# Kernel optimization log

Hardware: AMD Instinct MI355X
Metric: run time of the kernel (lower is better)

Reference implementation:

```python
import jax, jax.numpy as jnp
import numpy as np

D = 1024
H = 16
HD = D // H

def setup_inputs() -> dict:
    key = jax.random.key(0)
    ks = jax.random.split(key, 5)
    scale = 1.0 / np.sqrt(D)
    x = jax.random.normal(ks[0], (2, 2048, D), dtype=jnp.float32)
    W_qkv = jax.random.uniform(ks[1], (D, 3 * D), minval=-scale, maxval=scale, dtype=jnp.float32)
    b_qkv = jax.random.uniform(ks[2], (3 * D,), minval=-scale, maxval=scale, dtype=jnp.float32)
    W_out = jax.random.uniform(ks[3], (D, D), minval=-scale, maxval=scale, dtype=jnp.float32)
    b_out = jax.random.uniform(ks[4], (D,), minval=-scale, maxval=scale, dtype=jnp.float32)
    return {"x": x, "W_qkv": W_qkv, "b_qkv": b_qkv, "W_out": W_out, "b_out": b_out}

def reference(x, W_qkv, b_qkv, W_out, b_out):
    B, S, _ = x.shape
    qkv = x @ W_qkv + b_qkv  # [B,S,3D]
    qkv = qkv.reshape(B, S, 3, H, HD).transpose(2, 0, 3, 1, 4)  # [3,B,H,S,HD]
    q, k, v = qkv[0], qkv[1], qkv[2]
    scores = jnp.einsum('bhsd,bhtd->bhst', q, k) / jnp.sqrt(jnp.float32(HD))
    probs = jax.nn.softmax(scores, axis=-1)
    attn = jnp.einsum('bhst,bhtd->bhsd', probs, v)  # [B,H,S,HD]
    attn = attn.transpose(0, 2, 1, 3).reshape(B, S, D)
    return attn @ W_out + b_out
```

## Files before the change

### kernel.cpp

```cpp
#include <hip/hip_runtime.h>


typedef short bf16x8 __attribute__((ext_vector_type(8)));
typedef short bf16x4 __attribute__((ext_vector_type(4)));
typedef float f32x4 __attribute__((ext_vector_type(4)));

#if __has_builtin(__builtin_amdgcn_mfma_f32_16x16x16_bf16)
#define MFMA16(a, b, c) __builtin_amdgcn_mfma_f32_16x16x16_bf16(a, b, c, 0, 0, 0)
#else
#define MFMA16(a, b, c) __builtin_amdgcn_mfma_f32_16x16x16bf16_1k(a, b, c, 0, 0, 0)
#endif

__device__ __forceinline__ unsigned short f2bf(float f) {
  unsigned u = __float_as_uint(f);
  u = (u + 0x7fffu + ((u >> 16) & 1u)) >> 16;
  return (unsigned short)u;
}
__device__ __forceinline__ unsigned pack_bf2(float lo, float hi) {
  unsigned a = __float_as_uint(lo) + 0x8000u;
  unsigned b = __float_as_uint(hi) + 0x8000u;
  return __builtin_amdgcn_perm(b, a, 0x07060302);
}
__device__ __forceinline__ void load_lds16(const unsigned short* g, unsigned short* l) {
  __builtin_amdgcn_global_load_lds(
      (const __attribute__((address_space(1))) void*)g,
      (__attribute__((address_space(3))) void*)l, 16, 0, 0);
}

__global__ __launch_bounds__(256) void prep(
    const float* __restrict__ x, unsigned short* __restrict__ x_bf,
    const float* __restrict__ W_qkv, unsigned short* __restrict__ Wqkv_t,
    const float* __restrict__ W_out, unsigned short* __restrict__ Wout_t)
{
  const int tid = threadIdx.x;
  if (blockIdx.z == 2) {
    const int bid = blockIdx.y * 48 + blockIdx.x;
    const int n = 4096 * 1024;
    for (int i = bid * 2048 + tid * 8; i < n; i += 768 * 2048) {
      float4 f0 = *(const float4*)(x + i);
      float4 f1 = *(const float4*)(x + i + 4);
      union { unsigned short u[8]; uint4 v; } pk;
      pk.u[0] = f2bf(f0.x); pk.u[1] = f2bf(f0.y); pk.u[2] = f2bf(f0.z); pk.u[3] = f2bf(f0.w);
      pk.u[4] = f2bf(f1.x); pk.u[5] = f2bf(f1.y); pk.u[6] = f2bf(f1.z); pk.u[7] = f2bf(f1.w);
      *(uint4*)(x_bf + i) = pk.v;
    }
    return;
  }
  const float* in = (blockIdx.z == 0) ? W_qkv : W_out;
  unsigned short* out = (blockIdx.z == 0) ? Wqkv_t : Wout_t;
  const int R = 1024;
  const int C = (blockIdx.z == 0) ? 3072 : 1024;
  const int c0 = blockIdx.x * 64;
  if (c0 >= C) return;
  __shared__ float tile[64][65];
  const int r0 = blockIdx.y * 64;
  {
    const int rr = tid >> 4;
    const int cc = (tid & 15) * 4;
#pragma unroll
    for (int it = 0; it < 4; ++it) {
      float4 f = *(const float4*)&in[(size_t)(r0 + rr + 16 * it) * C + c0 + cc];
      tile[rr + 16 * it][cc + 0] = f.x;
      tile[rr + 16 * it][cc + 1] = f.y;
      tile[rr + 16 * it][cc + 2] = f.z;
      tile[rr + 16 * it][cc + 3] = f.w;
    }
  }
  __syncthreads();
  {
    const int cr = tid >> 2;
    const int rk = (tid & 3) * 16;
    union { unsigned short u[16]; uint4 v[2]; } pk;
#pragma unroll
    for (int j = 0; j < 16; ++j) pk.u[j] = f2bf(tile[rk + j][cr]);
    uint4* dst = (uint4*)&out[(size_t)(c0 + cr) * R + r0 + rk];
    dst[0] = pk.v[0];
    dst[1] = pk.v[1];
  }
}

template <int MODE>
__global__ __launch_bounds__(256) void gemm_mfma(
    const unsigned short* __restrict__ A,
    const unsigned short* __restrict__ Bt,
    const float* __restrict__ bias,
    void* __restrict__ Cout, unsigned short* __restrict__ vT,
    int M, int N, int K, int ldc)
{
  __shared__ unsigned short As[128][32];
  __shared__ unsigned short Bs[128][32];
  const int tid = threadIdx.x;
  const int wave = tid >> 6, lane = tid & 63;
  const int l16 = lane & 15, quad = lane >> 4;
  const int m0 = blockIdx.y * 128, n0 = blockIdx.x * 128;
  const int wm = (wave & 1) * 64, wn = (wave >> 1) * 64;
  const int lr = lane >> 2;
  const int lc = (lane & 3) * 8;

  f32x4 acc[4][4] = {};

  for (int k0 = 0; k0 < K; k0 += 32) {
    __syncthreads();
    load_lds16(&A [(size_t)(m0 + 16 * wave + lr) * K + k0 + lc],      &As[16 * wave][0]);
    load_lds16(&A [(size_t)(m0 + 64 + 16 * wave + lr) * K + k0 + lc], &As[64 + 16 * wave][0]);
    load_lds16(&Bt[(size_t)(n0 + 16 * wave + lr) * K + k0 + lc],      &Bs[16 * wave][0]);
    load_lds16(&Bt[(size_t)(n0 + 64 + 16 * wave + lr) * K + k0 + lc], &Bs[64 + 16 * wave][0]);
    __syncthreads();

    bf16x8 af[4], bfr[4];
#pragma unroll
    for (int mi = 0; mi < 4; ++mi)
      af[mi] = *(const bf16x8*)&As[wm + 16 * mi + l16][quad * 8];
#pragma unroll
    for (int ni = 0; ni < 4; ++ni)
      bfr[ni] = *(const bf16x8*)&Bs[wn + 16 * ni + l16][quad * 8];
#pragma unroll
    for (int mi = 0; mi < 4; ++mi)
#pragma unroll
      for (int ni = 0; ni < 4; ++ni)
        acc[mi][ni] = __builtin_amdgcn_mfma_f32_16x16x32_bf16(
            af[mi], bfr[ni], acc[mi][ni], 0, 0, 0);
  }

  const float SCQ = 0.18033688f;
#pragma unroll
  for (int ni = 0; ni < 4; ++ni) {
    const int colb = n0 + wn + 16 * ni;
    const int col = colb + l16;
    const float bv = bias[col];
    if (MODE == 0) {
#pragma unroll
      for (int mi = 0; mi < 4; ++mi)
#pragma unroll
        for (int i = 0; i < 4; ++i) {
          const int row = m0 + wm + 16 * mi + quad * 4 + i;
          ((float*)Cout)[(size_t)row * ldc + col] = acc[mi][ni][i] + bv;
        }
    } else if (colb < 1024) {
#pragma unroll
      for (int mi = 0; mi < 4; ++mi)
#pragma unroll
        for (int i = 0; i < 4; ++i) {
          const int row = m0 + wm + 16 * mi + quad * 4 + i;
          ((unsigned short*)Cout)[(size_t)row * ldc + col] = f2bf((acc[mi][ni][i] + bv) * SCQ);
        }
    } else if (colb < 2048) {
#pragma unroll
      for (int mi = 0; mi < 4; ++mi)
#pragma unroll
        for (int i = 0; i < 4; ++i) {
          const int row = m0 + wm + 16 * mi + quad * 4 + i;
          ((unsigned short*)Cout)[(size_t)row * ldc + col] = f2bf(acc[mi][ni][i] + bv);
        }
    } else {
      const int h = (col - 2048) >> 6, d = col & 63;
#pragma unroll
      for (int mi = 0; mi < 4; ++mi) {
        const int row = m0 + wm + 16 * mi + quad * 4;
        const int bb = row >> 11, t = row & 2047;
        unsigned short* dst = &vT[((size_t)(bb * 16 + h) * 64 + d) * 2048 + t];
        *(unsigned*)(dst)     = pack_bf2(acc[mi][ni][0] + bv, acc[mi][ni][1] + bv);
        *(unsigned*)(dst + 2) = pack_bf2(acc[mi][ni][2] + bv, acc[mi][ni][3] + bv);
      }
    }
  }
}

__global__ __launch_bounds__(256, 2) void attn_mfma(
    const unsigned short* __restrict__ qk,
    const unsigned short* __restrict__ vT,
    unsigned short* __restrict__ attn_out)
{
  __shared__ unsigned short Ks[2][4096];
  __shared__ unsigned short Vs[2][4096];

  const int tid = threadIdx.x;
  const int wave = tid >> 6, lane = tid & 63;
  const int l16 = lane & 15, quad = lane >> 4;
  const int bh = blockIdx.y, b = bh >> 4, h = bh & 15;
  const int s0 = blockIdx.x * 128 + wave * 32;

  const unsigned short* qb = qk + (size_t)(b * 2048) * 2048 + h * 64;
  const unsigned short* kb = qb + 1024;
  const unsigned short* vb = vT + (size_t)bh * 64 * 2048;

  const int srow = lane >> 3;
  const int schunk = ((lane & 7) ^ srow) * 8;
  const int r0a = wave * 16;
  const unsigned short* kg0 = kb + (size_t)(r0a + srow) * 2048 + schunk;
  const unsigned short* kg1 = kg0 + (size_t)8 * 2048;
  const unsigned short* vg0 = vb + (size_t)(r0a + srow) * 2048 + schunk;
  const unsigned short* vg1 = vg0 + (size_t)8 * 2048;
  const int wd0 = r0a * 64 + lane * 8;
  const int wd1 = (r0a + 8) * 64 + lane * 8;

  uint4 kr0 = *(const uint4*)(kg0);
  uint4 kr1 = *(const uint4*)(kg1);
  uint4 vr0 = *(const uint4*)(vg0);
  uint4 vr1 = *(const uint4*)(vg1);
  *(uint4*)&Ks[0][wd0] = kr0;  *(uint4*)&Ks[0][wd1] = kr1;
  *(uint4*)&Vs[0][wd0] = vr0;  *(uint4*)&Vs[0][wd1] = vr1;
  kr0 = *(const uint4*)(kg0 + (size_t)64 * 2048);
  kr1 = *(const uint4*)(kg1 + (size_t)64 * 2048);
  vr0 = *(const uint4*)(vg0 + 64);
  vr1 = *(const uint4*)(vg1 + 64);

  bf16x8 qf[2][2];
#pragma unroll
  for (int mt = 0; mt < 2; ++mt)
#pragma unroll
    for (int ks = 0; ks < 2; ++ks)
      qf[mt][ks] = *(const bf16x8*)&qb[(size_t)(s0 + 16 * mt + l16) * 2048 + 32 * ks + quad * 8];

  f32x4 O[2][4] = {};
  f32x4 lacc[2] = {};
  const bf16x4 ones4 = {(short)0x3F80, (short)0x3F80, (short)0x3F80, (short)0x3F80};
  const int sw = l16 & 7;
  const int h2 = quad >> 1, h1 = (quad & 1) * 4;

  __syncthreads();

  for (int it = 0; it < 32; ++it) {
    const int cur = it & 1;

    bf16x8 kf[4][2];
#pragma unroll
    for (int nt = 0; nt < 4; ++nt) {
      const int rb = (16 * nt + l16) * 64;
      kf[nt][0] = *(const bf16x8*)&Ks[cur][rb + ((quad ^ sw) * 8)];
      kf[nt][1] = *(const bf16x8*)&Ks[cur][rb + (((4 + quad) ^ sw) * 8)];
    }

    f32x4 sf[4][2];
#pragma unroll
    for (int nt = 0; nt < 4; ++nt)
#pragma unroll
      for (int mt = 0; mt < 2; ++mt) {
        f32x4 c = {0.0f, 0.0f, 0.0f, 0.0f};
        c = __builtin_amdgcn_mfma_f32_16x16x32_bf16(kf[nt][0], qf[mt][0], c, 0, 0, 0);
        c = __builtin_amdgcn_mfma_f32_16x16x32_bf16(kf[nt][1], qf[mt][1], c, 0, 0, 0);
        sf[nt][mt] = c;
      }

    if (it < 31) {
      *(uint4*)&Ks[cur ^ 1][wd0] = kr0;
      *(uint4*)&Ks[cur ^ 1][wd1] = kr1;
      *(uint4*)&Vs[cur ^ 1][wd0] = vr0;
      *(uint4*)&Vs[cur ^ 1][wd1] = vr1;
      if (it < 30) {
        const size_t ko = (size_t)(it + 2) * 64 * 2048;
        kr0 = *(const uint4*)(kg0 + ko);
        kr1 = *(const uint4*)(kg1 + ko);
        vr0 = *(const uint4*)(vg0 + (it + 2) * 64);
        vr1 = *(const uint4*)(vg1 + (it + 2) * 64);
      }
    }

    bf16x4 vf[4][4];
#pragma unroll
    for (int nd = 0; nd < 4; ++nd) {
      const int rb = (16 * nd + l16) * 64;
#pragma unroll
      for (int c = 0; c < 4; ++c)
        vf[nd][c] = *(const bf16x4*)&Vs[cur][rb + (((2 * c + h2) ^ sw) * 8 + h1)];
    }

    bf16x4 pp[2][4];
#pragma unroll
    for (int mt = 0; mt < 2; ++mt)
#pragma unroll
      for (int nt = 0; nt < 4; ++nt) {
        const float p0 = __builtin_amdgcn_exp2f(sf[nt][mt][0]);
        const float p1 = __builtin_amdgcn_exp2f(sf[nt][mt][1]);
        const float p2 = __builtin_amdgcn_exp2f(sf[nt][mt][2]);
        const float p3 = __builtin_amdgcn_exp2f(sf[nt][mt][3]);
        uint2 w;
        w.x = pack_bf2(p0, p1);
        w.y = pack_bf2(p2, p3);
        pp[mt][nt] = *(bf16x4*)&w;
      }

#pragma unroll
    for (int c = 0; c < 4; ++c)
#pragma unroll
      for (int mt = 0; mt < 2; ++mt) {
        lacc[mt] = MFMA16(ones4, pp[mt][c], lacc[mt]);
#pragma unroll
        for (int nd = 0; nd < 4; ++nd)
          O[mt][nd] = MFMA16(vf[nd][c], pp[mt][c], O[mt][nd]);
      }

    __syncthreads();
  }

#pragma unroll
  for (int mt = 0; mt < 2; ++mt) {
    const float inv = 1.0f / lacc[mt][0];
    const size_t row = (size_t)(b * 2048 + s0 + 16 * mt + l16);
#pragma unroll
    for (int nd = 0; nd < 4; ++nd) {
      uint2 w;
      w.x = pack_bf2(O[mt][nd][0] * inv, O[mt][nd][1] * inv);
      w.y = pack_bf2(O[mt][nd][2] * inv, O[mt][nd][3] * inv);
      *(uint2*)&attn_out[row * 1024 + h * 64 + 16 * nd + quad * 4] = w;
    }
  }
}

extern "C" void kernel_launch(void* const* d_in, const int* in_sizes, int n_in,
                              void* d_out, int out_size, void* d_ws, size_t ws_size,
                              hipStream_t stream) {
  const float* x     = (const float*)d_in[0];
  const float* W_qkv = (const float*)d_in[1];
  const float* b_qkv = (const float*)d_in[2];
  const float* W_out = (const float*)d_in[3];
  const float* b_out = (const float*)d_in[4];
  float* out = (float*)d_out;

  char* ws = (char*)d_ws;
  const size_t MB = 1048576;
  unsigned short* Wout_t = (unsigned short*)(ws);
  unsigned short* qk_bf  = (unsigned short*)(ws + 2 * MB);
  unsigned short* vT     = (unsigned short*)(ws + 18 * MB);
  unsigned short* attn_b = (unsigned short*)(ws + 26 * MB);
  unsigned short* x_bf   = (unsigned short*)(ws + 34 * MB);
  unsigned short* Wqkv_t = (unsigned short*)(ws + 42 * MB);

  prep<<<dim3(48, 16, 3), 256, 0, stream>>>(x, x_bf, W_qkv, Wqkv_t, W_out, Wout_t);

  gemm_mfma<1><<<dim3(24, 32), 256, 0, stream>>>(x_bf, Wqkv_t, b_qkv, qk_bf, vT,
                                                 4096, 3072, 1024, 2048);
  attn_mfma<<<dim3(16, 32), 256, 0, stream>>>(qk_bf, vT, attn_b);
  gemm_mfma<0><<<dim3(8, 32), 256, 0, stream>>>(attn_b, Wout_t, b_out, out, nullptr,
                                                4096, 1024, 1024, 1024);
}
```

Baseline: 196.0 us.

## Use single-wave attention blocks without barriers and smaller-tile output GEMM

Rewrites the attention kernel so each block is one wavefront handling 64 query rows. That removes __syncthreads and the XOR swizzle in favour of a padded LDS layout (stride 72), and each lane now loads the whole K/V tile itself. The output projection gets its own kernel with 64x128 tiles to launch more blocks, and the QKV GEMM is specialised with K fixed. The trade-off is much lower occupancy per block (64 threads, launch bounds with one block) and higher register pressure from 16 prefetch registers and larger accumulators, while removing block barriers and raising grid parallelism.

```diff
diff --git a/kernel.cpp b/kernel.cpp
--- a/kernel.cpp
+++ b/kernel.cpp
@@ -10,6 +10,7 @@
 #else
 #define MFMA16(a, b, c) __builtin_amdgcn_mfma_f32_16x16x16bf16_1k(a, b, c, 0, 0, 0)
 #endif
+#define MFMA32(a, b, c) __builtin_amdgcn_mfma_f32_16x16x32_bf16(a, b, c, 0, 0, 0)
 
 __device__ __forceinline__ unsigned short f2bf(float f) {
   unsigned u = __float_as_uint(f);
@@ -79,13 +80,12 @@
   }
 }
 
-template <int MODE>
-__global__ __launch_bounds__(256) void gemm_mfma(
+__global__ __launch_bounds__(256) void gemm_qkv(
     const unsigned short* __restrict__ A,
     const unsigned short* __restrict__ Bt,
     const float* __restrict__ bias,
-    void* __restrict__ Cout, unsigned short* __restrict__ vT,
-    int M, int N, int K, int ldc)
+    unsigned short* __restrict__ qkc,
+    unsigned short* __restrict__ vT)
 {
   __shared__ unsigned short As[128][32];
   __shared__ unsigned short Bs[128][32];
@@ -96,6 +96,7 @@
   const int wm = (wave & 1) * 64, wn = (wave >> 1) * 64;
   const int lr = lane >> 2;
   const int lc = (lane & 3) * 8;
+  const int K = 1024;
 
   f32x4 acc[4][4] = {};
 
@@ -118,8 +119,7 @@
     for (int mi = 0; mi < 4; ++mi)
 #pragma unroll
       for (int ni = 0; ni < 4; ++ni)
-        acc[mi][ni] = __builtin_amdgcn_mfma_f32_16x16x32_bf16(
-            af[mi], bfr[ni], acc[mi][ni], 0, 0, 0);
+        acc[mi][ni] = MFMA32(af[mi], bfr[ni], acc[mi][ni]);
   }
 
   const float SCQ = 0.18033688f;
@@ -128,29 +128,21 @@
     const int colb = n0 + wn + 16 * ni;
     const int col = colb + l16;
     const float bv = bias[col];
-    if (MODE == 0) {
+    if (colb < 1024) {
 #pragma unroll
       for (int mi = 0; mi < 4; ++mi)
 #pragma unroll
         for (int i = 0; i < 4; ++i) {
           const int row = m0 + wm + 16 * mi + quad * 4 + i;
-          ((float*)Cout)[(size_t)row * ldc + col] = acc[mi][ni][i] + bv;
+          qkc[(size_t)row * 2048 + col] = f2bf((acc[mi][ni][i] + bv) * SCQ);
         }
-    } else if (colb < 1024) {
+    } else if (colb < 2048) {
 #pragma unroll
       for (int mi = 0; mi < 4; ++mi)
 #pragma unroll
         for (int i = 0; i < 4; ++i) {
           const int row = m0 + wm + 16 * mi + quad * 4 + i;
-          ((unsigned short*)Cout)[(size_t)row * ldc + col] = f2bf((acc[mi][ni][i] + bv) * SCQ);
-        }
-    } else if (colb < 2048) {
-#pragma unroll
-      for (int mi = 0; mi < 4; ++mi)
-#pragma unroll
-        for (int i = 0; i < 4; ++i) {
-          const int row = m0 + wm + 16 * mi + quad * 4 + i;
-          ((unsigned short*)Cout)[(size_t)row * ldc + col] = f2bf(acc[mi][ni][i] + bv);
+          qkc[(size_t)row * 2048 + col] = f2bf(acc[mi][ni][i] + bv);
         }
     } else {
       const int h = (col - 2048) >> 6, d = col & 63;
@@ -166,59 +158,56 @@
   }
 }
 
-__global__ __launch_bounds__(256, 2) void attn_mfma(
+__global__ __launch_bounds__(64, 1) void attn_mfma(
     const unsigned short* __restrict__ qk,
     const unsigned short* __restrict__ vT,
     unsigned short* __restrict__ attn_out)
 {
-  __shared__ unsigned short Ks[2][4096];
-  __shared__ unsigned short Vs[2][4096];
-
-  const int tid = threadIdx.x;
-  const int wave = tid >> 6, lane = tid & 63;
+  __shared__ unsigned short Ks[2][4608];
+  __shared__ unsigned short Vs[2][4608];
+
+  const int lane = threadIdx.x;
   const int l16 = lane & 15, quad = lane >> 4;
   const int bh = blockIdx.y, b = bh >> 4, h = bh & 15;
-  const int s0 = blockIdx.x * 128 + wave * 32;
+  const int s0 = blockIdx.x * 64;
 
   const unsigned short* qb = qk + (size_t)(b * 2048) * 2048 + h * 64;
   const unsigned short* kb = qb + 1024;
   const unsigned short* vb = vT + (size_t)bh * 64 * 2048;
 
   const int srow = lane >> 3;
-  const int schunk = ((lane & 7) ^ srow) * 8;
-  const int r0a = wave * 16;
-  const unsigned short* kg0 = kb + (size_t)(r0a + srow) * 2048 + schunk;
-  const unsigned short* kg1 = kg0 + (size_t)8 * 2048;
-  const unsigned short* vg0 = vb + (size_t)(r0a + srow) * 2048 + schunk;
-  const unsigned short* vg1 = vg0 + (size_t)8 * 2048;
-  const int wd0 = r0a * 64 + lane * 8;
-  const int wd1 = (r0a + 8) * 64 + lane * 8;
-
-  uint4 kr0 = *(const uint4*)(kg0);
-  uint4 kr1 = *(const uint4*)(kg1);
-  uint4 vr0 = *(const uint4*)(vg0);
-  uint4 vr1 = *(const uint4*)(vg1);
-  *(uint4*)&Ks[0][wd0] = kr0;  *(uint4*)&Ks[0][wd1] = kr1;
-  *(uint4*)&Vs[0][wd0] = vr0;  *(uint4*)&Vs[0][wd1] = vr1;
-  kr0 = *(const uint4*)(kg0 + (size_t)64 * 2048);
-  kr1 = *(const uint4*)(kg1 + (size_t)64 * 2048);
-  vr0 = *(const uint4*)(vg0 + 64);
-  vr1 = *(const uint4*)(vg1 + 64);
-
-  bf16x8 qf[2][2];
-#pragma unroll
-  for (int mt = 0; mt < 2; ++mt)
+  const int sc = (lane & 7) * 8;
+  const unsigned short* kg = kb + (size_t)srow * 2048 + sc;
+  const unsigned short* vg = vb + (size_t)srow * 2048 + sc;
+  const int wbase = srow * 72 + sc;
+
+  uint4 kr[8], vr[8];
+#pragma unroll
+  for (int j = 0; j < 8; ++j) {
+    kr[j] = *(const uint4*)(kg + (size_t)(8 * j) * 2048);
+    vr[j] = *(const uint4*)(vg + (size_t)(8 * j) * 2048);
+  }
+#pragma unroll
+  for (int j = 0; j < 8; ++j) {
+    *(uint4*)&Ks[0][wbase + j * 576] = kr[j];
+    *(uint4*)&Vs[0][wbase + j * 576] = vr[j];
+  }
+#pragma unroll
+  for (int j = 0; j < 8; ++j) {
+    kr[j] = *(const uint4*)(kg + (size_t)(64 + 8 * j) * 2048);
+    vr[j] = *(const uint4*)(vg + 64 + (size_t)(8 * j) * 2048);
+  }
+
+  bf16x8 qf[4][2];
+#pragma unroll
+  for (int mt = 0; mt < 4; ++mt)
 #pragma unroll
     for (int ks = 0; ks < 2; ++ks)
       qf[mt][ks] = *(const bf16x8*)&qb[(size_t)(s0 + 16 * mt + l16) * 2048 + 32 * ks + quad * 8];
 
-  f32x4 O[2][4] = {};
-  f32x4 lacc[2] = {};
+  f32x4 O[4][4] = {};
+  f32x4 lacc[4] = {};
   const bf16x4 ones4 = {(short)0x3F80, (short)0x3F80, (short)0x3F80, (short)0x3F80};
-  const int sw = l16 & 7;
-  const int h2 = quad >> 1, h1 = (quad & 1) * 4;
-
-  __syncthreads();
 
   for (int it = 0; it < 32; ++it) {
     const int cur = it & 1;
@@ -226,48 +215,50 @@
     bf16x8 kf[4][2];
 #pragma unroll
     for (int nt = 0; nt < 4; ++nt) {
-      const int rb = (16 * nt + l16) * 64;
-      kf[nt][0] = *(const bf16x8*)&Ks[cur][rb + ((quad ^ sw) * 8)];
-      kf[nt][1] = *(const bf16x8*)&Ks[cur][rb + (((4 + quad) ^ sw) * 8)];
-    }
-
-    f32x4 sf[4][2];
+      const int rb = (16 * nt + l16) * 72;
+      kf[nt][0] = *(const bf16x8*)&Ks[cur][rb + quad * 8];
+      kf[nt][1] = *(const bf16x8*)&Ks[cur][rb + 32 + quad * 8];
+    }
+
+    f32x4 sf[4][4];
 #pragma unroll
     for (int nt = 0; nt < 4; ++nt)
 #pragma unroll
-      for (int mt = 0; mt < 2; ++mt) {
+      for (int mt = 0; mt < 4; ++mt) {
         f32x4 c = {0.0f, 0.0f, 0.0f, 0.0f};
-        c = __builtin_amdgcn_mfma_f32_16x16x32_bf16(kf[nt][0], qf[mt][0], c, 0, 0, 0);
-        c = __builtin_amdgcn_mfma_f32_16x16x32_bf16(kf[nt][1], qf[mt][1], c, 0, 0, 0);
+        c = MFMA32(kf[nt][0], qf[mt][0], c);
+        c = MFMA32(kf[nt][1], qf[mt][1], c);
         sf[nt][mt] = c;
       }
 
+    bf16x4 vf[4][4];
+#pragma unroll
+    for (int nd = 0; nd < 4; ++nd) {
+      const int rb = (16 * nd + l16) * 72;
+#pragma unroll
+      for (int c = 0; c < 4; ++c)
+        vf[nd][c] = *(const bf16x4*)&Vs[cur][rb + c * 16 + quad * 4];
+    }
+
     if (it < 31) {
-      *(uint4*)&Ks[cur ^ 1][wd0] = kr0;
-      *(uint4*)&Ks[cur ^ 1][wd1] = kr1;
-      *(uint4*)&Vs[cur ^ 1][wd0] = vr0;
-      *(uint4*)&Vs[cur ^ 1][wd1] = vr1;
+#pragma unroll
+      for (int j = 0; j < 8; ++j) {
+        *(uint4*)&Ks[cur ^ 1][wbase + j * 576] = kr[j];
+        *(uint4*)&Vs[cur ^ 1][wbase + j * 576] = vr[j];
+      }
       if (it < 30) {
-        const size_t ko = (size_t)(it + 2) * 64 * 2048;
-        kr0 = *(const uint4*)(kg0 + ko);
-        kr1 = *(const uint4*)(kg1 + ko);
-        vr0 = *(const uint4*)(vg0 + (it + 2) * 64);
-        vr1 = *(const uint4*)(vg1 + (it + 2) * 64);
-      }
-    }
-
-    bf16x4 vf[4][4];
-#pragma unroll
-    for (int nd = 0; nd < 4; ++nd) {
-      const int rb = (16 * nd + l16) * 64;
-#pragma unroll
-      for (int c = 0; c < 4; ++c)
-        vf[nd][c] = *(const bf16x4*)&Vs[cur][rb + (((2 * c + h2) ^ sw) * 8 + h1)];
-    }
-
-    bf16x4 pp[2][4];
-#pragma unroll
-    for (int mt = 0; mt < 2; ++mt)
+        const size_t t0 = (size_t)(it + 2) * 64;
+#pragma unroll
+        for (int j = 0; j < 8; ++j) {
+          kr[j] = *(const uint4*)(kg + (t0 + 8 * j) * 2048);
+          vr[j] = *(const uint4*)(vg + t0 + (size_t)(8 * j) * 2048);
+        }
+      }
+    }
+
+    bf16x4 pp[4][4];
+#pragma unroll
+    for (int mt = 0; mt < 4; ++mt)
 #pragma unroll
       for (int nt = 0; nt < 4; ++nt) {
         const float p0 = __builtin_amdgcn_exp2f(sf[nt][mt][0]);
@@ -283,18 +274,16 @@
 #pragma unroll
     for (int c = 0; c < 4; ++c)
 #pragma unroll
-      for (int mt = 0; mt < 2; ++mt) {
+      for (int mt = 0; mt < 4; ++mt) {
         lacc[mt] = MFMA16(ones4, pp[mt][c], lacc[mt]);
 #pragma unroll
         for (int nd = 0; nd < 4; ++nd)
           O[mt][nd] = MFMA16(vf[nd][c], pp[mt][c], O[mt][nd]);
       }
-
-    __syncthreads();
-  }
-
-#pragma unroll
-  for (int mt = 0; mt < 2; ++mt) {
+  }
+
+#pragma unroll
+  for (int mt = 0; mt < 4; ++mt) {
     const float inv = 1.0f / lacc[mt][0];
     const size_t row = (size_t)(b * 2048 + s0 + 16 * mt + l16);
 #pragma unroll
@@ -304,6 +293,59 @@
       w.y = pack_bf2(O[mt][nd][2] * inv, O[mt][nd][3] * inv);
       *(uint2*)&attn_out[row * 1024 + h * 64 + 16 * nd + quad * 4] = w;
     }
+  }
+}
+
+__global__ __launch_bounds__(256) void gemm_out(
+    const unsigned short* __restrict__ A,
+    const unsigned short* __restrict__ Bt,
+    const float* __restrict__ bias,
+    float* __restrict__ C)
+{
+  __shared__ unsigned short As[64][32];
+  __shared__ unsigned short Bs[128][32];
+  const int tid = threadIdx.x;
+  const int wave = tid >> 6, lane = tid & 63;
+  const int l16 = lane & 15, quad = lane >> 4;
+  const int m0 = blockIdx.y * 64, n0 = blockIdx.x * 128;
+  const int wn = wave * 32;
+  const int lr = lane >> 2;
+  const int lc = (lane & 3) * 8;
+
+  f32x4 acc[4][2] = {};
+
+  for (int k0 = 0; k0 < 1024; k0 += 32) {
+    __syncthreads();
+    load_lds16(&A [(size_t)(m0 + 16 * wave + lr) * 1024 + k0 + lc],      &As[16 * wave][0]);
+    load_lds16(&Bt[(size_t)(n0 + 32 * wave + lr) * 1024 + k0 + lc],      &Bs[32 * wave][0]);
+    load_lds16(&Bt[(size_t)(n0 + 32 * wave + 16 + lr) * 1024 + k0 + lc], &Bs[32 * wave + 16][0]);
+    __syncthreads();
+
+    bf16x8 af[4], bfr[2];
+#pragma unroll
+    for (int mi = 0; mi < 4; ++mi)
+      af[mi] = *(const bf16x8*)&As[16 * mi + l16][quad * 8];
+#pragma unroll
+    for (int ni = 0; ni < 2; ++ni)
+      bfr[ni] = *(const bf16x8*)&Bs[wn + 16 * ni + l16][quad * 8];
+#pragma unroll
+    for (int mi = 0; mi < 4; ++mi)
+#pragma unroll
+      for (int ni = 0; ni < 2; ++ni)
+        acc[mi][ni] = MFMA32(af[mi], bfr[ni], acc[mi][ni]);
+  }
+
+#pragma unroll
+  for (int ni = 0; ni < 2; ++ni) {
+    const int col = n0 + wn + 16 * ni + l16;
+    const float bv = bias[col];
+#pragma unroll
+    for (int mi = 0; mi < 4; ++mi)
+#pragma unroll
+      for (int i = 0; i < 4; ++i) {
+        const int row = m0 + 16 * mi + quad * 4 + i;
+        C[(size_t)row * 1024 + col] = acc[mi][ni][i] + bv;
+      }
   }
 }
 
@@ -328,9 +370,7 @@
 
   prep<<<dim3(48, 16, 3), 256, 0, stream>>>(x, x_bf, W_qkv, Wqkv_t, W_out, Wout_t);
 
-  gemm_mfma<1><<<dim3(24, 32), 256, 0, stream>>>(x_bf, Wqkv_t, b_qkv, qk_bf, vT,
-                                                 4096, 3072, 1024, 2048);
-  attn_mfma<<<dim3(16, 32), 256, 0, stream>>>(qk_bf, vT, attn_b);
-  gemm_mfma<0><<<dim3(8, 32), 256, 0, stream>>>(attn_b, Wout_t, b_out, out, nullptr,
-                                                4096, 1024, 1024, 1024);
-}
+  gemm_qkv<<<dim3(24, 32), 256, 0, stream>>>(x_bf, Wqkv_t, b_qkv, qk_bf, vT);
+  attn_mfma<<<dim3(32, 32), 64, 0, stream>>>(qk_bf, vT, attn_b);
+  gemm_out<<<dim3(8, 64), 256, 0, stream>>>(attn_b, Wout_t, b_out, out);
+}
```

Measured after the change: 502.5 us. 156% more time.
